# Optimization experiments

Hardware: AMD Instinct MI355X
Metric: run time of the kernel (lower is better)

Reference implementation:

```python
import jax, jax.numpy as jnp
import numpy as np

N_NODES = 50000


def _gcn_conv(x, edge_index, W, b):
    # x: [N, F_in], edge_index: [2, E] (with self-loops already added)
    n = x.shape[0]
    src, dst = edge_index[0], edge_index[1]
    h = x @ W  # [N, F_out] transform first (as in PyG GCNConv)
    deg = jax.ops.segment_sum(jnp.ones_like(dst, dtype=h.dtype), dst, num_segments=n)
    dinv = jax.lax.rsqrt(jnp.maximum(deg, 1.0))  # self-loops guarantee deg >= 1
    norm = dinv[src] * dinv[dst]  # [E]
    msg = h[src] * norm[:, None]  # [E, F_out] gather + scale
    out = jax.ops.segment_sum(msg, dst, num_segments=n)  # scatter-add to targets
    return out + b


def setup_inputs() -> dict:
    key = jax.random.key(0)
    k1, k2, k3, k4 = jax.random.split(key, 4)
    num_features, hidden, num_classes = 128, 128, 16
    n, e = N_NODES, 800000
    x = jax.random.normal(k1, (n, num_features), dtype=jnp.float32)
    edge_index = jax.random.randint(k2, (2, e), 0, n, dtype=jnp.int64)
    # add self-loops (PyG GCNConv default add_self_loops=True)
    loops = jnp.arange(n, dtype=jnp.int64)
    edge_index = jnp.concatenate([edge_index, jnp.stack([loops, loops])], axis=1)
    s1 = 1.0 / np.sqrt(num_features)
    s2 = 1.0 / np.sqrt(hidden)
    W1 = jax.random.uniform(k3, (num_features, hidden), jnp.float32, -s1, s1)
    b1 = jnp.zeros((hidden,), jnp.float32)
    W2 = jax.random.uniform(k4, (hidden, num_classes), jnp.float32, -s2, s2)
    b2 = jnp.zeros((num_classes,), jnp.float32)
    return {"x": x, "edge_index": edge_index, "W1": W1, "b1": b1, "W2": W2, "b2": b2}


def reference(x, edge_index, W1, b1, W2, b2):
    h = jax.nn.relu(_gcn_conv(x, edge_index, W1, b1))
    # dropout is identity in eval mode (deterministic reference)
    h = _gcn_conv(h, edge_index, W2, b2)
    return jax.nn.log_softmax(h, axis=1)
```

## Files before the change

kernel.cpp:

```cpp
#include <hip/hip_runtime.h>


typedef unsigned int uint32;
typedef unsigned short u16;
typedef __attribute__((ext_vector_type(8))) short bf16x8;
typedef __attribute__((ext_vector_type(4))) float f32x4;

#define NBMAX 1024
#define CHUNK 2048
#define EH 8192

__device__ inline u16 bf16rn(float f) {
    unsigned u = __float_as_uint(f);
    return (u16)((u + 0x7fffu + ((u >> 16) & 1u)) >> 16);
}

__device__ inline void bffma(float2& a, float w, uint32 u) {
    a.x = fmaf(w, __uint_as_float(u << 16), a.x);
    a.y = fmaf(w, __uint_as_float(u & 0xffff0000u), a.y);
}

__global__ __launch_bounds__(256) void k_combo(
    const float* __restrict__ x, const float* __restrict__ W1,
    const int* __restrict__ dstv, int* __restrict__ gh,
    u16* __restrict__ h, int N, int E, int NB, int ntile)
{
    __shared__ __align__(16) unsigned char smem[128 * 136 * 2];
    int t = threadIdx.x;

    if ((int)blockIdx.x >= ntile) {
        int* hl = (int*)smem;
        int hb = blockIdx.x - ntile;
        int e0 = hb * EH, e1 = min(e0 + EH, E);
        for (int i = t; i < NB; i += 256) hl[i] = 0;
        __syncthreads();
        for (int e = e0 + t; e < e1; e += 256)
            atomicAdd(&hl[dstv[e] >> 8], 1);
        __syncthreads();
        for (int i = t; i < NB; i += 256) {
            int c = hl[i];
            if (c) atomicAdd(&gh[i], c);
        }
        return;
    }

    u16* Wl = (u16*)smem;
    const float4* Wg4 = (const float4*)W1;
    for (int g = t; g < 128 * 32; g += 256) {
        int k = g >> 5, n4 = (g & 31) * 4;
        float4 v = Wg4[g];
        Wl[(n4 + 0) * 136 + k] = bf16rn(v.x);
        Wl[(n4 + 1) * 136 + k] = bf16rn(v.y);
        Wl[(n4 + 2) * 136 + k] = bf16rn(v.z);
        Wl[(n4 + 3) * 136 + k] = bf16rn(v.w);
    }
    __syncthreads();

    int wave = t >> 6, lane = t & 63;
    int quad = lane >> 4, ln = lane & 15;
    int rowbase = blockIdx.x * 64 + wave * 16;
    int node = rowbase + ln;
    int rclamp = min(node, N - 1);

    f32x4 acc[8];
    #pragma unroll
    for (int ct = 0; ct < 8; ++ct) acc[ct] = (f32x4){0.f, 0.f, 0.f, 0.f};

    #pragma unroll
    for (int q = 0; q < 4; ++q) {
        const float4* xr = (const float4*)(x + (size_t)rclamp * 128 + q * 32 + quad * 8);
        float4 a0 = xr[0], a1 = xr[1];
        bf16x8 xfr;
        xfr[0] = (short)bf16rn(a0.x); xfr[1] = (short)bf16rn(a0.y);
        xfr[2] = (short)bf16rn(a0.z); xfr[3] = (short)bf16rn(a0.w);
        xfr[4] = (short)bf16rn(a1.x); xfr[5] = (short)bf16rn(a1.y);
        xfr[6] = (short)bf16rn(a1.z); xfr[7] = (short)bf16rn(a1.w);
        #pragma unroll
        for (int ct = 0; ct < 8; ++ct) {
            bf16x8 wfr = *(const bf16x8*)&Wl[(ct * 16 + ln) * 136 + q * 32 + quad * 8];
            acc[ct] = __builtin_amdgcn_mfma_f32_16x16x32_bf16(wfr, xfr, acc[ct], 0, 0, 0);
        }
    }
    if (node < N) {
        u16* hp = h + (size_t)node * 128 + quad * 4;
        #pragma unroll
        for (int ct = 0; ct < 8; ++ct) {
            uint2 v;
            v.x = (uint32)bf16rn(acc[ct][0]) | ((uint32)bf16rn(acc[ct][1]) << 16);
            v.y = (uint32)bf16rn(acc[ct][2]) | ((uint32)bf16rn(acc[ct][3]) << 16);
            *(uint2*)(hp + ct * 16) = v;
        }
    }
}

__global__ __launch_bounds__(1024) void k_scanB(
    const int* __restrict__ gh, int* __restrict__ bbase,
    int* __restrict__ bfill, int NB, int E)
{
    __shared__ int wsum[16];
    int t = threadIdx.x;
    int lane = t & 63, wv = t >> 6;
    int v = (t < NB) ? gh[t] : 0;
    int sc = v;
    #pragma unroll
    for (int off = 1; off < 64; off <<= 1) {
        int u = __shfl_up(sc, off);
        if (lane >= off) sc += u;
    }
    if (lane == 63) wsum[wv] = sc;
    __syncthreads();
    if (wv == 0 && lane < 16) {
        int b = wsum[lane];
        int bs = b;
        #pragma unroll
        for (int off = 1; off < 16; off <<= 1) {
            int u = __shfl_up(bs, off);
            if (lane >= off) bs += u;
        }
        wsum[lane] = bs - b;
    }
    __syncthreads();
    int incl = sc + wsum[wv];
    if (t < NB) {
        bbase[t] = incl - v;
        bfill[t] = 0;
    }
    if (t == 0) bbase[NB] = E;
}

__global__ __launch_bounds__(512) void k_partition(
    const int* __restrict__ src, const int* __restrict__ dstv,
    const int* __restrict__ bbase, int* __restrict__ bfill,
    uint32* __restrict__ tmp, int E, int NB)
{
    __shared__ int cntL[NBMAX];
    __shared__ int baseL[NBMAX];
    int t = threadIdx.x;
    int e0 = blockIdx.x * CHUNK;
    int e1 = min(e0 + CHUNK, E);
    for (int i = t; i < NB; i += 512) cntL[i] = 0;
    __syncthreads();
    for (int e = e0 + t; e < e1; e += 512)
        atomicAdd(&cntL[dstv[e] >> 8], 1);
    __syncthreads();
    for (int i = t; i < NB; i += 512) {
        int cc = cntL[i];
        baseL[i] = cc ? bbase[i] + atomicAdd(&bfill[i], cc) : 0;
        cntL[i] = 0;
    }
    __syncthreads();
    for (int e = e0 + t; e < e1; e += 512) {
        int sv = src[e], d = dstv[e];
        int b = d >> 8;
        int r = atomicAdd(&cntL[b], 1);
        tmp[baseL[b] + r] = (uint32)sv | ((uint32)(d & 255) << 16);
    }
}

__global__ __launch_bounds__(1024) void k_bsort(
    const uint32* __restrict__ tmp, const int* __restrict__ bbase,
    u16* __restrict__ ssrc, int* __restrict__ rs,
    float* __restrict__ dinv, int N)
{
    __shared__ int cnt[256];
    __shared__ int ofs[256];
    int t = threadIdx.x;
    int b = blockIdx.x;
    int base = bbase[b];
    int endb = bbase[b + 1];
    int node0 = b << 8;

    if (t < 256) cnt[t] = 0;
    __syncthreads();
    for (int i = base + t; i < endb; i += 1024)
        atomicAdd(&cnt[(tmp[i] >> 16) & 255], 1);
    __syncthreads();
    int v = (t < 256) ? cnt[t] : 0;
    __syncthreads();
    for (int off = 1; off < 256; off <<= 1) {
        int u = (t >= off && t < 256) ? cnt[t - off] : 0;
        __syncthreads();
        if (t < 256) cnt[t] += u;
        __syncthreads();
    }
    if (t < 256) {
        int node = node0 + t;
        if (node < N) {
            dinv[node] = rsqrtf(fmaxf((float)v, 1.0f));
            rs[node] = base + cnt[t];
        }
        ofs[t] = base + cnt[t] - v;
    }
    __syncthreads();
    for (int i = base + t; i < endb; i += 1024) {
        uint32 rec = tmp[i];
        int pos = atomicAdd(&ofs[(rec >> 16) & 255], 1);
        ssrc[pos] = (u16)(rec & 0xffffu);
    }
}

__global__ __launch_bounds__(256) void k_pullg(
    const int* __restrict__ rs, const u16* __restrict__ ssrc,
    const float* __restrict__ dinv, const uint2* __restrict__ h,
    const float* __restrict__ b1, const float* __restrict__ W2,
    u16* __restrict__ h2, int N)
{
    __shared__ float W2T[16 * 132];
    __shared__ float rowbuf[8 * 132];
    int t = threadIdx.x;

    for (int g = t; g < 2048; g += 256) {
        int k = g >> 4, f = g & 15;
        W2T[f * 132 + k] = W2[g];
    }

    int wave = t >> 6, lane = t & 63;
    int sub = lane >> 5;
    int rl = lane & 31;
    int rowbase = blockIdx.x * 8;
    int n = rowbase + wave * 2 + sub;
    bool valid = (n < N);
    int nc = valid ? n : 0;
    int start = valid ? ((nc == 0) ? 0 : rs[nc - 1]) : 0;
    int len   = valid ? (rs[nc] - start) : 0;
    float dn  = valid ? dinv[nc] : 0.f;
    int lenMax = max(len, __shfl_xor(len, 32));

    float2 aA[4], aB[4];
    #pragma unroll
    for (int k = 0; k < 4; ++k) {
        aA[k] = (float2){0.f, 0.f};
        aB[k] = (float2){0.f, 0.f};
    }

    for (int tt = 0; tt < lenMax; tt += 8) {
        int s[8];
        uint2 u[8];
        float w[8];
        #pragma unroll
        for (int k = 0; k < 8; ++k) {
            bool act = (tt + k) < len;
            int jj = act ? (start + tt + k) : 0;
            s[k] = (int)ssrc[jj];
            w[k] = act ? 1.f : 0.f;
        }
        #pragma unroll
        for (int k = 0; k < 8; ++k)
            u[k] = h[(size_t)s[k] * 32 + rl];
        #pragma unroll
        for (int k = 0; k < 8; ++k)
            w[k] *= dinv[s[k]];
        #pragma unroll
        for (int k = 0; k < 8; ++k) {
            bffma(aA[k & 3], w[k], u[k].x);
            bffma(aB[k & 3], w[k], u[k].y);
        }
    }

    {
        int r = wave * 2 + sub;
        float4 bb = ((const float4*)b1)[rl];
        float4 v;
        v.x = fmaxf(fmaf(dn, (aA[0].x + aA[1].x) + (aA[2].x + aA[3].x), bb.x), 0.f);
        v.y = fmaxf(fmaf(dn, (aA[0].y + aA[1].y) + (aA[2].y + aA[3].y), bb.y), 0.f);
        v.z = fmaxf(fmaf(dn, (aB[0].x + aB[1].x) + (aB[2].x + aB[3].x), bb.z), 0.f);
        v.w = fmaxf(fmaf(dn, (aB[0].y + aB[1].y) + (aB[2].y + aB[3].y), bb.w), 0.f);
        ((float4*)rowbuf)[r * 33 + rl] = v;
    }
    __syncthreads();

    if (t < 128) {
        int f = t & 15, r = t >> 4;
        const float4* W4 = (const float4*)W2T;
        const float4* rb4 = (const float4*)rowbuf;
        float acc = 0.f;
        #pragma unroll 8
        for (int k4 = 0; k4 < 32; ++k4) {
            float4 w = W4[f * 33 + k4];
            float4 xv = rb4[r * 33 + k4];
            acc = fmaf(xv.x, w.x, acc);
            acc = fmaf(xv.y, w.y, acc);
            acc = fmaf(xv.z, w.z, acc);
            acc = fmaf(xv.w, w.w, acc);
        }
        int rn = rowbase + r;
        if (rn < N) h2[(size_t)rn * 16 + f] = bf16rn(acc);
    }
}

__global__ __launch_bounds__(256) void k_pull2(
    const int* __restrict__ rs, const u16* __restrict__ ssrc,
    const float* __restrict__ dinv, const uint32* __restrict__ h2,
    const float* __restrict__ b2, float* __restrict__ out, int N)
{
    int idx = blockIdx.x * 256 + threadIdx.x;
    int n = idx >> 3;
    if (n >= N) return;
    int c = idx & 7;
    int start = (n == 0) ? 0 : rs[n - 1];
    int len = rs[n] - start;
    float dn = dinv[n];

    float2 a[4];
    #pragma unroll
    for (int k = 0; k < 4; ++k) a[k] = (float2){0.f, 0.f};

    for (int tt = 0; tt < len; tt += 4) {
        int s[4];
        uint32 u[4];
        float w[4];
        #pragma unroll
        for (int k = 0; k < 4; ++k) {
            bool act = (tt + k) < len;
            int jj = act ? (start + tt + k) : 0;
            s[k] = (int)ssrc[jj];
            w[k] = act ? 1.f : 0.f;
        }
        #pragma unroll
        for (int k = 0; k < 4; ++k)
            u[k] = h2[(size_t)s[k] * 8 + c];
        #pragma unroll
        for (int k = 0; k < 4; ++k)
            w[k] *= dn * dinv[s[k]];
        #pragma unroll
        for (int k = 0; k < 4; ++k)
            bffma(a[k], w[k], u[k]);
    }

    float acc0 = (a[0].x + a[1].x) + (a[2].x + a[3].x);
    float acc1 = (a[0].y + a[1].y) + (a[2].y + a[3].y);
    float v0 = acc0 + b2[2 * c];
    float v1 = acc1 + b2[2 * c + 1];
    float m = fmaxf(v0, v1);
    #pragma unroll
    for (int off = 1; off < 8; off <<= 1) m = fmaxf(m, __shfl_xor(m, off));
    float s = expf(v0 - m) + expf(v1 - m);
    #pragma unroll
    for (int off = 1; off < 8; off <<= 1) s += __shfl_xor(s, off);
    float ls = logf(s);
    float2 r = {v0 - m - ls, v1 - m - ls};
    ((float2*)out)[(size_t)n * 8 + c] = r;
}

extern "C" void kernel_launch(void* const* d_in, const int* in_sizes, int n_in,
                              void* d_out, int out_size, void* d_ws, size_t ws_size,
                              hipStream_t stream) {
    const float* x  = (const float*)d_in[0];
    const int*   ei = (const int*)d_in[1];
    const float* W1 = (const float*)d_in[2];
    const float* b1 = (const float*)d_in[3];
    const float* W2 = (const float*)d_in[4];
    const float* b2 = (const float*)d_in[5];
    float* outp = (float*)d_out;

    const int E = in_sizes[1] / 2;
    const int N = in_sizes[0] / 128;
    const int NB = (N + 255) >> 8;
    const int NH = (E + EH - 1) / EH;
    const int ntile = (N + 63) / 64;
    const int* src  = ei;
    const int* dstv = ei + E;

    const int Npad = (N + 255) & ~255;
    const int Epad = (E + 255) & ~255;
    int*   gh    = (int*)d_ws;
    int*   bbase = gh + NBMAX;
    int*   bfill = bbase + NBMAX + 256;
    int*   rs    = bfill + NBMAX;
    float* dinv  = (float*)(rs + Npad);
    uint32* tmp  = (uint32*)(dinv + Npad);
    u16*   ssrc  = (u16*)(tmp + Epad);
    uintptr_t hp = ((uintptr_t)(ssrc + Epad) + 255) & ~(uintptr_t)255;
    u16*   h     = (u16*)hp;
    u16*   h2    = h + (size_t)Npad * 128;

    hipMemsetAsync(gh, 0, NBMAX * sizeof(int), stream);
    k_combo<<<ntile + NH, 256, 0, stream>>>(x, W1, dstv, gh, h, N, E, NB, ntile);
    k_scanB<<<1, 1024, 0, stream>>>(gh, bbase, bfill, NB, E);
    k_partition<<<(E + CHUNK - 1) / CHUNK, 512, 0, stream>>>(src, dstv, bbase,
                                                             bfill, tmp, E, NB);
    k_bsort<<<NB, 1024, 0, stream>>>(tmp, bbase, ssrc, rs, dinv, N);
    k_pullg<<<(N + 7) / 8, 256, 0, stream>>>(rs, ssrc, dinv, (const uint2*)h,
                                             b1, W2, h2, N);
    k_pull2<<<(N * 8 + 255) / 256, 256, 0, stream>>>(rs, ssrc, dinv,
                                                     (const uint32*)h2, b2, outp, N);
}
```

Measured before the change: 172.1 us.

## Pack source index with bf16 source weight and use one wave per node

Adds a small pass that packs each sorted edge's source index with a bf16-rounded dinv[src] into one 32-bit record, reusing the tmp buffer. The layer-1 aggregation then assigns a full 64-lane wave per destination node instead of half a wave. Edge records are broadcast through readfirstlane, and the separate per-edge dinv gather is gone. Blocks grow to 512 threads, and the loop unroll drops from 8 to 4 edges. This costs an extra launch and pass over the edges, and the weights lose precision from bf16 rounding.

```diff
diff --git a/kernel.cpp b/kernel.cpp
--- a/kernel.cpp
+++ b/kernel.cpp
@@ -199,9 +199,19 @@
     }
 }
 
-__global__ __launch_bounds__(256) void k_pullg(
-    const int* __restrict__ rs, const u16* __restrict__ ssrc,
-    const float* __restrict__ dinv, const uint2* __restrict__ h,
+__global__ __launch_bounds__(256) void k_wgt(
+    const u16* __restrict__ ssrc, const float* __restrict__ dinv,
+    uint32* __restrict__ srec, int E)
+{
+    int i = blockIdx.x * 256 + threadIdx.x;
+    if (i >= E) return;
+    uint32 s = ssrc[i];
+    srec[i] = s | ((uint32)bf16rn(dinv[s]) << 16);
+}
+
+__global__ __launch_bounds__(512) void k_pullg(
+    const int* __restrict__ rs, const uint32* __restrict__ srec,
+    const float* __restrict__ dinv, const uint32* __restrict__ h32,
     const float* __restrict__ b1, const float* __restrict__ W2,
     u16* __restrict__ h2, int N)
 {
@@ -209,63 +219,53 @@
     __shared__ float rowbuf[8 * 132];
     int t = threadIdx.x;
 
-    for (int g = t; g < 2048; g += 256) {
+    for (int g = t; g < 2048; g += 512) {
         int k = g >> 4, f = g & 15;
         W2T[f * 132 + k] = W2[g];
     }
 
     int wave = t >> 6, lane = t & 63;
-    int sub = lane >> 5;
-    int rl = lane & 31;
-    int rowbase = blockIdx.x * 8;
-    int n = rowbase + wave * 2 + sub;
+    int n = blockIdx.x * 8 + wave;
     bool valid = (n < N);
     int nc = valid ? n : 0;
-    int start = valid ? ((nc == 0) ? 0 : rs[nc - 1]) : 0;
+    int start = (nc == 0) ? 0 : rs[nc - 1];
     int len   = valid ? (rs[nc] - start) : 0;
     float dn  = valid ? dinv[nc] : 0.f;
-    int lenMax = max(len, __shfl_xor(len, 32));
-
-    float2 aA[4], aB[4];
-    #pragma unroll
-    for (int k = 0; k < 4; ++k) {
-        aA[k] = (float2){0.f, 0.f};
-        aB[k] = (float2){0.f, 0.f};
-    }
-
-    for (int tt = 0; tt < lenMax; tt += 8) {
-        int s[8];
-        uint2 u[8];
-        float w[8];
-        #pragma unroll
-        for (int k = 0; k < 8; ++k) {
-            bool act = (tt + k) < len;
-            int jj = act ? (start + tt + k) : 0;
-            s[k] = (int)ssrc[jj];
-            w[k] = act ? 1.f : 0.f;
-        }
-        #pragma unroll
-        for (int k = 0; k < 8; ++k)
-            u[k] = h[(size_t)s[k] * 32 + rl];
-        #pragma unroll
-        for (int k = 0; k < 8; ++k)
-            w[k] *= dinv[s[k]];
-        #pragma unroll
-        for (int k = 0; k < 8; ++k) {
-            bffma(aA[k & 3], w[k], u[k].x);
-            bffma(aB[k & 3], w[k], u[k].y);
-        }
+
+    float2 a0 = {0.f, 0.f}, a1 = {0.f, 0.f}, a2 = {0.f, 0.f}, a3 = {0.f, 0.f};
+
+    for (int tt = 0; tt < len; tt += 4) {
+        int last = len - 1;
+        uint32 r0 = srec[start + tt];
+        uint32 r1 = srec[start + min(tt + 1, last)];
+        uint32 r2 = srec[start + min(tt + 2, last)];
+        uint32 r3 = srec[start + min(tt + 3, last)];
+        r0 = __builtin_amdgcn_readfirstlane(r0);
+        r1 = __builtin_amdgcn_readfirstlane(r1);
+        r2 = __builtin_amdgcn_readfirstlane(r2);
+        r3 = __builtin_amdgcn_readfirstlane(r3);
+        uint32 u0 = h32[(size_t)(r0 & 0xffffu) * 64 + lane];
+        uint32 u1 = h32[(size_t)(r1 & 0xffffu) * 64 + lane];
+        uint32 u2 = h32[(size_t)(r2 & 0xffffu) * 64 + lane];
+        uint32 u3 = h32[(size_t)(r3 & 0xffffu) * 64 + lane];
+        float w0 = __uint_as_float(r0 & 0xffff0000u);
+        float w1 = (tt + 1 < len) ? __uint_as_float(r1 & 0xffff0000u) : 0.f;
+        float w2 = (tt + 2 < len) ? __uint_as_float(r2 & 0xffff0000u) : 0.f;
+        float w3 = (tt + 3 < len) ? __uint_as_float(r3 & 0xffff0000u) : 0.f;
+        bffma(a0, w0, u0);
+        bffma(a1, w1, u1);
+        bffma(a2, w2, u2);
+        bffma(a3, w3, u3);
     }
 
     {
-        int r = wave * 2 + sub;
-        float4 bb = ((const float4*)b1)[rl];
-        float4 v;
-        v.x = fmaxf(fmaf(dn, (aA[0].x + aA[1].x) + (aA[2].x + aA[3].x), bb.x), 0.f);
-        v.y = fmaxf(fmaf(dn, (aA[0].y + aA[1].y) + (aA[2].y + aA[3].y), bb.y), 0.f);
-        v.z = fmaxf(fmaf(dn, (aB[0].x + aB[1].x) + (aB[2].x + aB[3].x), bb.z), 0.f);
-        v.w = fmaxf(fmaf(dn, (aB[0].y + aB[1].y) + (aB[2].y + aB[3].y), bb.w), 0.f);
-        ((float4*)rowbuf)[r * 33 + rl] = v;
+        float sx = (a0.x + a1.x) + (a2.x + a3.x);
+        float sy = (a0.y + a1.y) + (a2.y + a3.y);
+        float2 bb = ((const float2*)b1)[lane];
+        float2 v;
+        v.x = fmaxf(fmaf(dn, sx, bb.x), 0.f);
+        v.y = fmaxf(fmaf(dn, sy, bb.y), 0.f);
+        ((float2*)rowbuf)[wave * 66 + lane] = v;
     }
     __syncthreads();
 
@@ -283,7 +283,7 @@
             acc = fmaf(xv.z, w.z, acc);
             acc = fmaf(xv.w, w.w, acc);
         }
-        int rn = rowbase + r;
+        int rn = blockIdx.x * 8 + r;
         if (rn < N) h2[(size_t)rn * 16 + f] = bf16rn(acc);
     }
 }
@@ -380,8 +380,9 @@
     k_partition<<<(E + CHUNK - 1) / CHUNK, 512, 0, stream>>>(src, dstv, bbase,
                                                              bfill, tmp, E, NB);
     k_bsort<<<NB, 1024, 0, stream>>>(tmp, bbase, ssrc, rs, dinv, N);
-    k_pullg<<<(N + 7) / 8, 256, 0, stream>>>(rs, ssrc, dinv, (const uint2*)h,
-                                             b1, W2, h2, N);
+    k_wgt<<<(E + 255) / 256, 256, 0, stream>>>(ssrc, dinv, tmp, E);
+    k_pullg<<<(N + 7) / 8, 512, 0, stream>>>(rs, (const uint32*)tmp, dinv,
+                                             (const uint32*)h, b1, W2, h2, N);
     k_pull2<<<(N * 8 + 255) / 256, 256, 0, stream>>>(rs, ssrc, dinv,
                                                      (const uint32*)h2, b2, outp, N);
 }
```

After: 200.7 us. 1.17x slower.
